# Kernel tuning notes

Measured on AMD Instinct MI355X. Metric: run time of the kernel, lower is better.

Reference implementation:

```python
import jax, jax.numpy as jnp
import numpy as np

D_MODEL = 256
NUM_HEADS = 8
HEAD_DIM = D_MODEL // NUM_HEADS
B, L = 2, 2048


def setup_inputs() -> dict:
    key = jax.random.key(0)
    ks = jax.random.split(key, 16)
    s = 0.02
    return {
        "query": jax.random.normal(ks[0], (B, L, D_MODEL), jnp.float32),
        "key": jax.random.normal(ks[1], (B, L, D_MODEL), jnp.float32),
        "value": jax.random.normal(ks[2], (B, L, D_MODEL), jnp.float32),
        "struct_bias": jax.random.normal(ks[3], (B, NUM_HEADS, L, L), jnp.float32),
        "attn_mask": jax.random.normal(ks[4], (B, NUM_HEADS, L, L), jnp.float32),
        "Wq": jax.random.normal(ks[5], (D_MODEL, D_MODEL), jnp.float32) * s,
        "bq": jnp.zeros((D_MODEL,), jnp.float32),
        "Wk": jax.random.normal(ks[6], (D_MODEL, D_MODEL), jnp.float32) * s,
        "bk": jnp.zeros((D_MODEL,), jnp.float32),
        "Wv": jax.random.normal(ks[7], (D_MODEL, D_MODEL), jnp.float32) * s,
        "bv": jnp.zeros((D_MODEL,), jnp.float32),
        "Wo": jax.random.normal(ks[8], (D_MODEL, D_MODEL), jnp.float32) * s,
        "bo": jnp.zeros((D_MODEL,), jnp.float32),
    }


def reference(query, key, value, struct_bias, attn_mask,
              Wq, bq, Wk, bk, Wv, bv, Wo, bo):
    b, t, _ = query.shape
    # projections (torch Linear: x @ W.T + b)
    q = query @ Wq.T + bq
    k = key @ Wk.T + bk
    v = value @ Wv.T + bv
    # [B, H, L, Dh]
    q = q.reshape(b, t, NUM_HEADS, HEAD_DIM).transpose(0, 2, 1, 3)
    k = k.reshape(b, t, NUM_HEADS, HEAD_DIM).transpose(0, 2, 1, 3)
    v = v.reshape(b, t, NUM_HEADS, HEAD_DIM).transpose(0, 2, 1, 3)
    scale = 1.0 / np.sqrt(HEAD_DIM).astype(np.float32)
    scores = jnp.einsum("bhqd,bhkd->bhqk", q, k) * scale
    scores = scores + struct_bias + attn_mask
    attn_weights = jax.nn.softmax(scores, axis=-1)
    context = jnp.einsum("bhqk,bhkd->bhqd", attn_weights, v)
    context = context.transpose(0, 2, 1, 3).reshape(b, t, D_MODEL)
    output = context @ Wo.T + bo
    return (output, attn_weights)
```

## Files before the change

### kernel.cpp

```cpp
#include <hip/hip_runtime.h>

typedef __bf16 bf16x8 __attribute__((ext_vector_type(8)));
typedef short  s16x8  __attribute__((ext_vector_type(8)));
typedef float  f32x4  __attribute__((ext_vector_type(4)));

#define MFMA16(a,b,c) __builtin_amdgcn_mfma_f32_16x16x32_bf16((a),(b),(c),0,0,0)

static constexpr float SCALE = 0.17677669529663687f;

__device__ __forceinline__ unsigned short f2b(float f){
  __bf16 h = (__bf16)f;
  return __builtin_bit_cast(unsigned short, h);
}
__device__ __forceinline__ bf16x8 ldfrag(const unsigned short* p){
  s16x8 v = *(const s16x8*)p;
  return __builtin_bit_cast(bf16x8, v);
}
__device__ __forceinline__ bf16x8 cvt8(const float* p){
  f32x4 a = *(const f32x4*)p;
  f32x4 b = *(const f32x4*)(p+4);
  bf16x8 r;
  r[0]=(__bf16)a[0]; r[1]=(__bf16)a[1]; r[2]=(__bf16)a[2]; r[3]=(__bf16)a[3];
  r[4]=(__bf16)b[0]; r[5]=(__bf16)b[1]; r[6]=(__bf16)b[2]; r[7]=(__bf16)b[3];
  return r;
}

__global__ __launch_bounds__(256) void proj_kernel(
    const float* __restrict__ xq, const float* __restrict__ xk, const float* __restrict__ xv,
    const float* __restrict__ Wq, const float* __restrict__ bq,
    const float* __restrict__ Wk, const float* __restrict__ bk,
    const float* __restrict__ Wv, const float* __restrict__ bv,
    unsigned short* __restrict__ qo, unsigned short* __restrict__ ko,
    unsigned short* __restrict__ vT)
{
  const int z = blockIdx.z;
  const float* x    = (z==0) ? xq : (z==1 ? xk : xv);
  const float* W    = (z==0) ? Wq : (z==1 ? Wk : Wv);
  const float* bias = (z==0) ? bq : (z==1 ? bk : bv);
  const int tid = threadIdx.x, w = tid>>6, l = tid&63;
  const int m0 = blockIdx.x*16;
  const int n0 = blockIdx.y*64 + w*16;
  const int ra = l&15, ko8 = (l>>4)*8;

  __shared__ unsigned short xs[16*264];
  #pragma unroll
  for(int i=0;i<4;++i){
    int chunk = tid + i*256;
    int row = chunk>>6, c4 = (chunk&63)*4;
    f32x4 v = *(const f32x4*)(x + (m0+row)*256 + c4);
    ushort4 u; u.x=f2b(v[0]); u.y=f2b(v[1]); u.z=f2b(v[2]); u.w=f2b(v[3]);
    *(ushort4*)(&xs[row*264 + c4]) = u;
  }
  __syncthreads();

  f32x4 acc = {0.f,0.f,0.f,0.f};
  #pragma unroll
  for(int kk=0;kk<8;++kk){
    int kb = kk*32 + ko8;
    bf16x8 a   = ldfrag(&xs[ra*264 + kb]);
    bf16x8 bfr = cvt8(W + (n0+ra)*256 + kb);
    acc = MFMA16(a, bfr, acc);
  }
  const int col = l&15;
  const int n = n0 + col;
  const float bval = bias[n];

  __shared__ float vt[4][16][17];
  if(z < 2){
    unsigned short* out = (z==0) ? qo : ko;
    #pragma unroll
    for(int r=0;r<4;++r){
      int R = (l>>4)*4 + r, m = m0 + R;
      float val = acc[r] + bval;
      if(z==0) val *= SCALE;
      int bidx = m>>11, ls = m&2047, hh = n>>5, dh = n&31;
      out[(((long)(bidx*8+hh))*2048 + ls)*32 + dh] = f2b(val);
    }
  } else {
    #pragma unroll
    for(int r=0;r<4;++r){
      int R = (l>>4)*4 + r;
      vt[w][R][col] = acc[r] + bval;
    }
    __syncthreads();
    int bidx = m0>>11, hh = n0>>5, dh0 = n0&31, bh = bidx*8 + hh;
    int lsc = m0 & 2047;
    int dloc = l>>2, kloc = (l&3)*4;
    ushort4 pk;
    pk.x = f2b(vt[w][kloc+0][dloc]);
    pk.y = f2b(vt[w][kloc+1][dloc]);
    pk.z = f2b(vt[w][kloc+2][dloc]);
    pk.w = f2b(vt[w][kloc+3][dloc]);
    *reinterpret_cast<ushort4*>(vT + ((long)(bh*32 + dh0 + dloc))*2048 + lsc + kloc) = pk;
  }
}

__global__ __launch_bounds__(512) void attn_kernel(
    const unsigned short* __restrict__ qbf, const unsigned short* __restrict__ kbf,
    const unsigned short* __restrict__ vT,
    const float* __restrict__ sbias, const float* __restrict__ amask,
    float* __restrict__ Pout, float* __restrict__ ctx)
{
  __shared__ float sS[8*2048];
  __shared__ float linv[8];

  const int tid = threadIdx.x, w = tid>>6, l = tid&63;
  const int q0 = blockIdx.x*8;
  const int h = blockIdx.y, b = blockIdx.z;
  const int bh = b*8 + h;
  const long qkbase = (long)bh*2048*32;
  const long bmbase = ((long)bh*2048 + q0)*2048;
  const long rowbase = bmbase + (long)w*2048;
  const int ws = w*256;
  const int col = l&15, ko8 = (l>>4)*8, rg = (l>>4)*4;
  const f32x4 zero = {0.f,0.f,0.f,0.f};

  f32x4 s[8];
  #pragma unroll
  for(int k=0;k<8;++k){
    long c = rowbase + k*256 + l*4;
    f32x4 b4 = __builtin_nontemporal_load((const f32x4*)(sbias + c));
    f32x4 m4 = __builtin_nontemporal_load((const f32x4*)(amask + c));
    s[k] = b4 + m4;
  }

  bf16x8 aq = ldfrag(qbf + qkbase + (long)(q0 + (col&7))*32 + ko8);
  #pragma unroll
  for(int t=0;t<16;++t){
    int key0 = ws + t*16;
    bf16x8 bk = ldfrag(kbf + qkbase + (long)(key0+col)*32 + ko8);
    f32x4 acc = MFMA16(aq, bk, zero);
    if(rg < 8){
      #pragma unroll
      for(int r=0;r<4;++r){
        int R = rg + r;
        sS[R*2048 + ((key0+col) ^ (R<<2))] = acc[r];
      }
    }
  }
  __syncthreads();

  const int swzw = w<<2;
  float m = -1e30f;
  #pragma unroll
  for(int k=0;k<8;++k){
    int c = k*256 + l*4;
    f32x4 v = *(const f32x4*)(&sS[w*2048 + (c ^ swzw)]);
    s[k][0]+=v[0]; s[k][1]+=v[1]; s[k][2]+=v[2]; s[k][3]+=v[3];
    m = fmaxf(m, fmaxf(fmaxf(s[k][0],s[k][1]), fmaxf(s[k][2],s[k][3])));
  }
  #pragma unroll
  for(int d=1;d<64;d<<=1) m = fmaxf(m, __shfl_xor(m, d));
  float sum = 0.f;
  #pragma unroll
  for(int k=0;k<8;++k){
    s[k][0]=__expf(s[k][0]-m); s[k][1]=__expf(s[k][1]-m);
    s[k][2]=__expf(s[k][2]-m); s[k][3]=__expf(s[k][3]-m);
    sum += (s[k][0]+s[k][1]) + (s[k][2]+s[k][3]);
  }
  #pragma unroll
  for(int d=1;d<64;d<<=1) sum += __shfl_xor(sum, d);
  const float li = 1.0f/sum;
  if(l==0) linv[w] = li;

  #pragma unroll
  for(int k=0;k<8;++k){
    int c = k*256 + l*4;
    f32x4 p; p[0]=s[k][0]*li; p[1]=s[k][1]*li; p[2]=s[k][2]*li; p[3]=s[k][3]*li;
    __builtin_nontemporal_store(p, (f32x4*)(Pout + rowbase + c));
    *(f32x4*)(&sS[w*2048 + (c ^ swzw)]) = s[k];
  }
  __syncthreads();

  f32x4 acc0 = zero, acc1 = zero;
  const long vbase = (long)bh*32*2048;
  const int prow = col&7;
  #pragma unroll
  for(int c=0;c<8;++c){
    int kb = ws + c*32 + ko8;
    f32x4 e0 = *(const f32x4*)(&sS[prow*2048 + ( kb    ^ (prow<<2))]);
    f32x4 e1 = *(const f32x4*)(&sS[prow*2048 + ((kb+4) ^ (prow<<2))]);
    bf16x8 pa;
    pa[0]=(__bf16)e0[0]; pa[1]=(__bf16)e0[1]; pa[2]=(__bf16)e0[2]; pa[3]=(__bf16)e0[3];
    pa[4]=(__bf16)e1[0]; pa[5]=(__bf16)e1[1]; pa[6]=(__bf16)e1[2]; pa[7]=(__bf16)e1[3];
    bf16x8 v0 = ldfrag(vT + vbase + (long)col*2048 + kb);
    bf16x8 v1 = ldfrag(vT + vbase + (long)(16+col)*2048 + kb);
    acc0 = MFMA16(pa, v0, acc0);
    acc1 = MFMA16(pa, v1, acc1);
  }
  __syncthreads();

  if(rg < 8){
    #pragma unroll
    for(int r=0;r<4;++r){
      int R = rg + r;
      sS[w*256 + R*32 + col]      = acc0[r];
      sS[w*256 + R*32 + 16 + col] = acc1[r];
    }
  }
  __syncthreads();
  if(tid < 256){
    int row = tid>>5, dh = tid&31;
    float ssum = 0.f;
    #pragma unroll
    for(int w2=0; w2<8; ++w2) ssum += sS[w2*256 + row*32 + dh];
    ctx[((long)b*2048 + q0 + row)*256 + h*32 + dh] = ssum * linv[row];
  }
}

__global__ __launch_bounds__(256) void oproj_kernel(
    float* __restrict__ out0, const float* __restrict__ Wo, const float* __restrict__ bo)
{
  __shared__ unsigned short lct[8*264];
  const int tid = threadIdx.x, w = tid>>6, l = tid&63;
  const int m0 = blockIdx.x*8;
  #pragma unroll
  for(int i=0;i<2;++i){
    int chunk = tid + i*256;
    int row = chunk>>6, c4 = (chunk&63)*4;
    f32x4 v = *(const f32x4*)(out0 + (m0+row)*256 + c4);
    ushort4 u; u.x=f2b(v[0]); u.y=f2b(v[1]); u.z=f2b(v[2]); u.w=f2b(v[3]);
    *(ushort4*)(&lct[row*264 + c4]) = u;
  }
  __syncthreads();
  const int col = l&15, ko8 = (l>>4)*8, rg = (l>>4)*4;
  const int arow = col&7;
  #pragma unroll
  for(int nt=0;nt<4;++nt){
    int n0 = w*64 + nt*16;
    f32x4 acc = {0.f,0.f,0.f,0.f};
    #pragma unroll
    for(int kk=0;kk<8;++kk){
      int kb = kk*32 + ko8;
      bf16x8 a   = ldfrag(&lct[arow*264 + kb]);
      bf16x8 bfr = cvt8(Wo + (n0+col)*256 + kb);
      acc = MFMA16(a, bfr, acc);
    }
    float bv = bo[n0+col];
    if(rg < 8){
      #pragma unroll
      for(int r=0;r<4;++r){
        out0[(m0+rg+r)*256 + n0+col] = acc[r] + bv;
      }
    }
  }
}

extern "C" void kernel_launch(void* const* d_in, const int* in_sizes, int n_in,
                              void* d_out, int out_size, void* d_ws, size_t ws_size,
                              hipStream_t stream)
{
  const float* query = (const float*)d_in[0];
  const float* key   = (const float*)d_in[1];
  const float* value = (const float*)d_in[2];
  const float* sbias = (const float*)d_in[3];
  const float* amask = (const float*)d_in[4];
  const float* Wq = (const float*)d_in[5];
  const float* bq = (const float*)d_in[6];
  const float* Wk = (const float*)d_in[7];
  const float* bk = (const float*)d_in[8];
  const float* Wv = (const float*)d_in[9];
  const float* bv = (const float*)d_in[10];
  const float* Wo = (const float*)d_in[11];
  const float* bo = (const float*)d_in[12];

  float* out0 = (float*)d_out;
  float* Pout = out0 + (size_t)2*2048*256;

  unsigned short* qbf = (unsigned short*)d_ws;
  unsigned short* kbf = qbf + (size_t)2*8*2048*32;
  unsigned short* vTb = kbf + (size_t)2*8*2048*32;

  proj_kernel<<<dim3(256,4,3), 256, 0, stream>>>(query,key,value,Wq,bq,Wk,bk,Wv,bv,qbf,kbf,vTb);
  attn_kernel<<<dim3(256,8,2), 512, 0, stream>>>(qbf,kbf,vTb,sbias,amask,Pout,out0);
  oproj_kernel<<<dim3(512), 256, 0, stream>>>(out0,Wo,bo);
}
```

Baseline: 244.4 us.

## Make attention persistent with 16-row tiles and prefetch next bias/mask rows

```diff
diff --git a/kernel.cpp b/kernel.cpp
--- a/kernel.cpp
+++ b/kernel.cpp
@@ -95,116 +95,131 @@
   }
 }
 
-__global__ __launch_bounds__(512) void attn_kernel(
+__global__ __launch_bounds__(1024) void attn_kernel(
     const unsigned short* __restrict__ qbf, const unsigned short* __restrict__ kbf,
     const unsigned short* __restrict__ vT,
     const float* __restrict__ sbias, const float* __restrict__ amask,
     float* __restrict__ Pout, float* __restrict__ ctx)
 {
-  __shared__ float sS[8*2048];
-  __shared__ float linv[8];
+  __shared__ float sS[16*2048];
+  __shared__ float linv[16];
 
   const int tid = threadIdx.x, w = tid>>6, l = tid&63;
-  const int q0 = blockIdx.x*8;
-  const int h = blockIdx.y, b = blockIdx.z;
-  const int bh = b*8 + h;
+  const int p = blockIdx.x;
+  const int bh = p >> 4;
+  const int qg = p & 15;
+  const int b = bh >> 3, h = bh & 7;
   const long qkbase = (long)bh*2048*32;
-  const long bmbase = ((long)bh*2048 + q0)*2048;
-  const long rowbase = bmbase + (long)w*2048;
-  const int ws = w*256;
+  const long vbase  = (long)bh*32*2048;
+  const int ws = w*128;
   const int col = l&15, ko8 = (l>>4)*8, rg = (l>>4)*4;
+  const int swzw = (w&7)<<2;
   const f32x4 zero = {0.f,0.f,0.f,0.f};
 
   f32x4 s[8];
-  #pragma unroll
-  for(int k=0;k<8;++k){
-    long c = rowbase + k*256 + l*4;
-    f32x4 b4 = __builtin_nontemporal_load((const f32x4*)(sbias + c));
-    f32x4 m4 = __builtin_nontemporal_load((const f32x4*)(amask + c));
-    s[k] = b4 + m4;
-  }
-
-  bf16x8 aq = ldfrag(qbf + qkbase + (long)(q0 + (col&7))*32 + ko8);
-  #pragma unroll
-  for(int t=0;t<16;++t){
-    int key0 = ws + t*16;
-    bf16x8 bk = ldfrag(kbf + qkbase + (long)(key0+col)*32 + ko8);
-    f32x4 acc = MFMA16(aq, bk, zero);
-    if(rg < 8){
+  {
+    const long rb0 = ((long)bh*2048 + qg*128 + w)*2048;
+    #pragma unroll
+    for(int k=0;k<8;++k){
+      long c = rb0 + k*256 + l*4;
+      f32x4 b4 = __builtin_nontemporal_load((const f32x4*)(sbias + c));
+      f32x4 m4 = __builtin_nontemporal_load((const f32x4*)(amask + c));
+      s[k] = b4 + m4;
+    }
+  }
+
+  for(int j=0;j<8;++j){
+    const int q0 = qg*128 + j*16;
+    const long bmbase = ((long)bh*2048 + q0)*2048;
+    const long rowbase = bmbase + (long)w*2048;
+
+    bf16x8 aq = ldfrag(qbf + qkbase + (long)(q0+col)*32 + ko8);
+    #pragma unroll
+    for(int t=0;t<8;++t){
+      int key0 = ws + t*16;
+      bf16x8 bk = ldfrag(kbf + qkbase + (long)(key0+col)*32 + ko8);
+      f32x4 acc = MFMA16(aq, bk, zero);
       #pragma unroll
       for(int r=0;r<4;++r){
         int R = rg + r;
-        sS[R*2048 + ((key0+col) ^ (R<<2))] = acc[r];
+        sS[R*2048 + ((key0+col) ^ ((R&7)<<2))] = acc[r];
       }
     }
-  }
-  __syncthreads();
-
-  const int swzw = w<<2;
-  float m = -1e30f;
-  #pragma unroll
-  for(int k=0;k<8;++k){
-    int c = k*256 + l*4;
-    f32x4 v = *(const f32x4*)(&sS[w*2048 + (c ^ swzw)]);
-    s[k][0]+=v[0]; s[k][1]+=v[1]; s[k][2]+=v[2]; s[k][3]+=v[3];
-    m = fmaxf(m, fmaxf(fmaxf(s[k][0],s[k][1]), fmaxf(s[k][2],s[k][3])));
-  }
-  #pragma unroll
-  for(int d=1;d<64;d<<=1) m = fmaxf(m, __shfl_xor(m, d));
-  float sum = 0.f;
-  #pragma unroll
-  for(int k=0;k<8;++k){
-    s[k][0]=__expf(s[k][0]-m); s[k][1]=__expf(s[k][1]-m);
-    s[k][2]=__expf(s[k][2]-m); s[k][3]=__expf(s[k][3]-m);
-    sum += (s[k][0]+s[k][1]) + (s[k][2]+s[k][3]);
-  }
-  #pragma unroll
-  for(int d=1;d<64;d<<=1) sum += __shfl_xor(sum, d);
-  const float li = 1.0f/sum;
-  if(l==0) linv[w] = li;
-
-  #pragma unroll
-  for(int k=0;k<8;++k){
-    int c = k*256 + l*4;
-    f32x4 p; p[0]=s[k][0]*li; p[1]=s[k][1]*li; p[2]=s[k][2]*li; p[3]=s[k][3]*li;
-    __builtin_nontemporal_store(p, (f32x4*)(Pout + rowbase + c));
-    *(f32x4*)(&sS[w*2048 + (c ^ swzw)]) = s[k];
-  }
-  __syncthreads();
-
-  f32x4 acc0 = zero, acc1 = zero;
-  const long vbase = (long)bh*32*2048;
-  const int prow = col&7;
-  #pragma unroll
-  for(int c=0;c<8;++c){
-    int kb = ws + c*32 + ko8;
-    f32x4 e0 = *(const f32x4*)(&sS[prow*2048 + ( kb    ^ (prow<<2))]);
-    f32x4 e1 = *(const f32x4*)(&sS[prow*2048 + ((kb+4) ^ (prow<<2))]);
-    bf16x8 pa;
-    pa[0]=(__bf16)e0[0]; pa[1]=(__bf16)e0[1]; pa[2]=(__bf16)e0[2]; pa[3]=(__bf16)e0[3];
-    pa[4]=(__bf16)e1[0]; pa[5]=(__bf16)e1[1]; pa[6]=(__bf16)e1[2]; pa[7]=(__bf16)e1[3];
-    bf16x8 v0 = ldfrag(vT + vbase + (long)col*2048 + kb);
-    bf16x8 v1 = ldfrag(vT + vbase + (long)(16+col)*2048 + kb);
-    acc0 = MFMA16(pa, v0, acc0);
-    acc1 = MFMA16(pa, v1, acc1);
-  }
-  __syncthreads();
-
-  if(rg < 8){
+    __syncthreads();
+
+    float m = -1e30f;
+    #pragma unroll
+    for(int k=0;k<8;++k){
+      int c = k*256 + l*4;
+      f32x4 v = *(const f32x4*)(&sS[w*2048 + (c ^ swzw)]);
+      s[k][0]+=v[0]; s[k][1]+=v[1]; s[k][2]+=v[2]; s[k][3]+=v[3];
+      m = fmaxf(m, fmaxf(fmaxf(s[k][0],s[k][1]), fmaxf(s[k][2],s[k][3])));
+    }
+    #pragma unroll
+    for(int d=1;d<64;d<<=1) m = fmaxf(m, __shfl_xor(m, d));
+    float sum = 0.f;
+    #pragma unroll
+    for(int k=0;k<8;++k){
+      s[k][0]=__expf(s[k][0]-m); s[k][1]=__expf(s[k][1]-m);
+      s[k][2]=__expf(s[k][2]-m); s[k][3]=__expf(s[k][3]-m);
+      sum += (s[k][0]+s[k][1]) + (s[k][2]+s[k][3]);
+    }
+    #pragma unroll
+    for(int d=1;d<64;d<<=1) sum += __shfl_xor(sum, d);
+    const float li = 1.0f/sum;
+    if(l==0) linv[w] = li;
+
+    #pragma unroll
+    for(int k=0;k<8;++k){
+      int c = k*256 + l*4;
+      f32x4 pv; pv[0]=s[k][0]*li; pv[1]=s[k][1]*li; pv[2]=s[k][2]*li; pv[3]=s[k][3]*li;
+      __builtin_nontemporal_store(pv, (f32x4*)(Pout + rowbase + c));
+      *(f32x4*)(&sS[w*2048 + (c ^ swzw)]) = s[k];
+    }
+
+    if(j < 7){
+      const long nb = rowbase + 16*2048;
+      #pragma unroll
+      for(int k=0;k<8;++k){
+        long c = nb + k*256 + l*4;
+        f32x4 b4 = __builtin_nontemporal_load((const f32x4*)(sbias + c));
+        f32x4 m4 = __builtin_nontemporal_load((const f32x4*)(amask + c));
+        s[k] = b4 + m4;
+      }
+    }
+    __syncthreads();
+
+    f32x4 acc0 = zero, acc1 = zero;
+    #pragma unroll
+    for(int c4=0;c4<4;++c4){
+      int kb = ws + c4*32 + ko8;
+      f32x4 e0 = *(const f32x4*)(&sS[col*2048 + ( kb    ^ ((col&7)<<2))]);
+      f32x4 e1 = *(const f32x4*)(&sS[col*2048 + ((kb+4) ^ ((col&7)<<2))]);
+      bf16x8 pa;
+      pa[0]=(__bf16)e0[0]; pa[1]=(__bf16)e0[1]; pa[2]=(__bf16)e0[2]; pa[3]=(__bf16)e0[3];
+      pa[4]=(__bf16)e1[0]; pa[5]=(__bf16)e1[1]; pa[6]=(__bf16)e1[2]; pa[7]=(__bf16)e1[3];
+      bf16x8 v0 = ldfrag(vT + vbase + (long)col*2048 + kb);
+      bf16x8 v1 = ldfrag(vT + vbase + (long)(16+col)*2048 + kb);
+      acc0 = MFMA16(pa, v0, acc0);
+      acc1 = MFMA16(pa, v1, acc1);
+    }
+    __syncthreads();
+
     #pragma unroll
     for(int r=0;r<4;++r){
       int R = rg + r;
-      sS[w*256 + R*32 + col]      = acc0[r];
-      sS[w*256 + R*32 + 16 + col] = acc1[r];
-    }
-  }
-  __syncthreads();
-  if(tid < 256){
-    int row = tid>>5, dh = tid&31;
-    float ssum = 0.f;
-    #pragma unroll
-    for(int w2=0; w2<8; ++w2) ssum += sS[w2*256 + row*32 + dh];
-    ctx[((long)b*2048 + q0 + row)*256 + h*32 + dh] = ssum * linv[row];
+      sS[w*512 + R*32 + col]      = acc0[r];
+      sS[w*512 + R*32 + 16 + col] = acc1[r];
+    }
+    __syncthreads();
+    if(tid < 512){
+      int row = tid>>5, dh = tid&31;
+      float ssum = 0.f;
+      #pragma unroll
+      for(int w2=0; w2<16; ++w2) ssum += sS[w2*512 + row*32 + dh];
+      ctx[((long)b*2048 + q0 + row)*256 + h*32 + dh] = ssum * linv[row];
+    }
+    __syncthreads();
   }
 }
 
@@ -272,6 +287,6 @@
   unsigned short* vTb = kbf + (size_t)2*8*2048*32;
 
   proj_kernel<<<dim3(256,4,3), 256, 0, stream>>>(query,key,value,Wq,bq,Wk,bk,Wv,bv,qbf,kbf,vTb);
-  attn_kernel<<<dim3(256,8,2), 512, 0, stream>>>(qbf,kbf,vTb,sbias,amask,Pout,out0);
+  attn_kernel<<<dim3(256), 1024, 0, stream>>>(qbf,kbf,vTb,sbias,amask,Pout,out0);
   oproj_kernel<<<dim3(512), 256, 0, stream>>>(out0,Wo,bo);
 }
```

Result: slower. 294.4 us (+20.5%).
